# Kernel tuning notes

Hardware: AMD Instinct MI355X
Metric: run time of the kernel (lower is better)

The kernel has to match this reference:

```python
import jax, jax.numpy as jnp
import numpy as np

B = 16384      # rays
H = 128        # field hidden dim


def setup_inputs() -> dict:
    key = jax.random.key(0)
    ks = jax.random.split(key, 8)
    origins = jax.random.normal(ks[0], (B, 3), dtype=jnp.float32)
    directions = jax.random.normal(ks[1], (B, 3), dtype=jnp.float32)
    directions = directions / jnp.linalg.norm(directions, axis=-1, keepdims=True)
    # Field: simple MLP 3 -> H -> H -> 4 (rgb + sigma)
    W1 = jax.random.normal(ks[2], (3, H), dtype=jnp.float32) * (1.0 / np.sqrt(3.0))
    b1 = jnp.zeros((H,), dtype=jnp.float32)
    W2 = jax.random.normal(ks[3], (H, H), dtype=jnp.float32) * (1.0 / np.sqrt(H))
    b2 = jnp.zeros((H,), dtype=jnp.float32)
    W3 = jax.random.normal(ks[4], (H, 4), dtype=jnp.float32) * (1.0 / np.sqrt(H))
    b3 = jnp.zeros((4,), dtype=jnp.float32)
    return {"origins": origins, "directions": directions,
            "W1": W1, "b1": b1, "W2": W2, "b2": b2, "W3": W3, "b3": b3,
            "near": 2, "far": 6, "num_samples": 64}


def _field(x, W1, b1, W2, b2, W3, b3):
    h = jax.nn.relu(x @ W1 + b1)
    h = jax.nn.relu(h @ W2 + b2)
    return h @ W3 + b3


def reference(origins, directions, W1, b1, W2, b2, W3, b3, near, far, num_samples):
    near = jnp.float32(near)
    far = jnp.float32(far)
    # 1. generate_samples: segment boundaries + midpoints along each ray
    depths = jnp.linspace(near, far, num_samples + 1)            # [S+1]
    midpoints = 0.5 * (depths[:-1] + depths[1:])                 # [S]
    # [B, S, 3] = origin + t * direction
    locs = origins[:, None, :] + midpoints[None, :, None] * directions[:, None, :]
    # 2. evaluate field
    f = _field(locs.reshape(-1, 3), W1, b1, W2, b2, W3, b3)
    f = f.reshape(origins.shape[0], num_samples, 4)
    # NOTE: source overwrites the sigmoid'd colors with raw outputs (faithful)
    colors = f[..., :3]                                          # [B, S, 3]
    sigma = f[..., 3]                                            # [B, S]
    # 3. alpha values
    delta = depths[1:] - depths[:-1]                             # [S]
    alphas = 1.0 - jnp.exp(-sigma * delta[None, :])              # [B, S]
    # 4. alpha compositing (black background)
    ones = jnp.ones_like(alphas[:, :1])
    transmittance = jnp.cumprod(jnp.concatenate([ones, 1.0 - alphas], axis=1), axis=1)[:, :-1]
    weights = alphas * transmittance                             # [B, S]
    radiance = jnp.sum(weights[..., None] * colors, axis=1)      # [B, 3]
    return radiance
```

## Files before the change

### kernel.cpp

```cpp
#include <hip/hip_runtime.h>


typedef _Float16 f16;
typedef __attribute__((ext_vector_type(2))) _Float16 h2v;
typedef __attribute__((ext_vector_type(8))) _Float16 half8;
typedef __attribute__((ext_vector_type(4))) float floatx4;

#define H 128
#define NS 64

static __device__ __forceinline__ h2v pkrtz(float a, float b) {
  return __builtin_bit_cast(h2v, __builtin_amdgcn_cvt_pkrtz(a, b));
}

__global__ void nerf_setup(const float* __restrict__ W2, const float* __restrict__ W3,
                           const float* __restrict__ b2,
                           f16* __restrict__ wsW2, f16* __restrict__ wsW3,
                           f16* __restrict__ wsB2) {
  int t = blockIdx.x * blockDim.x + threadIdx.x;
  if (t < 8192) {
    int j2 = t & 3, lane = (t >> 2) & 63, fid = t >> 8;
    int mtl = fid & 1, ks = (fid >> 1) & 3, wv = fid >> 3;
    int l16 = lane & 15;
    int k = ks * 32 + ((lane >> 4) * 8) + 2 * j2;
    int n = 32 * wv + (l16 >> 2) * 8 + mtl * 4 + (l16 & 3);
    wsW2[2 * t]     = (f16)W2[k * H + n];
    wsW2[2 * t + 1] = (f16)W2[(k + 1) * H + n];
  } else if (t < 9216) {
    int u = t - 8192;
    int j2 = u & 3, lane = (u >> 2) & 63, wv = u >> 8;
    int c = lane & 15;
    int k3 = 32 * wv + ((lane >> 4) * 8) + 2 * j2;
    wsW3[2 * u]     = (c < 4) ? (f16)W3[k3 * 4 + c]       : (f16)0.0f;
    wsW3[2 * u + 1] = (c < 4) ? (f16)W3[(k3 + 1) * 4 + c] : (f16)0.0f;
  } else if (t < 9344) {
    int i = t - 9216;
    wsB2[i] = (f16)b2[i];
  }
}

__global__ __launch_bounds__(256, 3) void nerf_main(
    const float* __restrict__ origins, const float* __restrict__ dirs,
    const float* __restrict__ W1, const float* __restrict__ b1,
    const float* __restrict__ b3,
    const f16* __restrict__ wsW2, const f16* __restrict__ wsW3,
    const f16* __restrict__ wsB2,
    float* __restrict__ out)
{
  __shared__ __align__(16) f16   popd[2][2][H];
  __shared__ __align__(16) float f_lds[4][128][4];

  const int t = threadIdx.x;
  const int w = t >> 6, lane = t & 63, quad = lane >> 4, l16 = lane & 15;
  const float delta = 4.0f / NS;

  const half8* w2f = (const half8*)wsW2;
  half8 aw[4][2];
  #pragma unroll
  for (int ks = 0; ks < 4; ++ks)
    #pragma unroll
    for (int mtl = 0; mtl < 2; ++mtl)
      aw[ks][mtl] = w2f[((w * 4 + ks) * 2 + mtl) * 64 + lane];
  const half8 w3 = ((const half8*)wsW3)[w * 64 + lane];
  h2v bk[4];
  {
    uint4 u = *(const uint4*)(wsB2 + 32 * w + quad * 8);
    bk[0] = __builtin_bit_cast(h2v, u.x);
    bk[1] = __builtin_bit_cast(h2v, u.y);
    bk[2] = __builtin_bit_cast(h2v, u.z);
    bk[3] = __builtin_bit_cast(h2v, u.w);
  }
  const float4 b3v = *(const float4*)b3;

  if (w < 2) {
    const int ray = blockIdx.x * 2 + w;
    const float o0 = origins[ray*3], o1 = origins[ray*3+1], o2 = origins[ray*3+2];
    const float d0 = dirs[ray*3],    d1 = dirs[ray*3+1],    d2 = dirs[ray*3+2];
    const int k0 = lane * 2;
    const float2 wr0 = *(const float2*)&W1[0*H + k0];
    const float2 wr1 = *(const float2*)&W1[1*H + k0];
    const float2 wr2 = *(const float2*)&W1[2*H + k0];
    const float2 bb  = *(const float2*)&b1[k0];
    float poa = fmaf(o2, wr2.x, fmaf(o1, wr1.x, fmaf(o0, wr0.x, bb.x)));
    float pob = fmaf(o2, wr2.y, fmaf(o1, wr1.y, fmaf(o0, wr0.y, bb.y)));
    float pda = fmaf(d2, wr2.x, fmaf(d1, wr1.x, d0 * wr0.x));
    float pdb = fmaf(d2, wr2.y, fmaf(d1, wr1.y, d0 * wr0.y));
    h2v po2; po2[0] = (f16)poa; po2[1] = (f16)pob;
    h2v pd2; pd2[0] = (f16)pda; pd2[1] = (f16)pdb;
    *(h2v*)&popd[w][0][k0] = po2;
    *(h2v*)&popd[w][1][k0] = pd2;
  }
  __syncthreads();

  h2v m2[8];
  #pragma unroll
  for (int nt = 0; nt < 8; ++nt) {
    const f16 m = (f16)(2.0f + ((nt & 3) * 16 + l16 + 0.5f) * delta);
    m2[nt][0] = m; m2[nt][1] = m;
  }

  floatx4 acc[2][8];
  #pragma unroll
  for (int nt = 0; nt < 8; ++nt) { acc[0][nt] = (floatx4)(0.0f); acc[1][nt] = (floatx4)(0.0f); }

  const h2v z2 = (h2v)(f16)0.0f;
  #pragma unroll
  for (int ks = 0; ks < 4; ++ks) {
    const half8 poA = *(const half8*)&popd[0][0][ks*32 + quad*8];
    const half8 pdA = *(const half8*)&popd[0][1][ks*32 + quad*8];
    const half8 poB = *(const half8*)&popd[1][0][ks*32 + quad*8];
    const half8 pdB = *(const half8*)&popd[1][1][ks*32 + quad*8];
    #pragma unroll
    for (int nt = 0; nt < 8; ++nt) {
      union { half8 v; h2v p[4]; } P, O, Hb;
      P.v = (nt < 4) ? pdA : pdB;
      O.v = (nt < 4) ? poA : poB;
      #pragma unroll
      for (int p2 = 0; p2 < 4; ++p2)
        Hb.p[p2] = __builtin_elementwise_max((h2v)(P.p[p2] * m2[nt] + O.p[p2]), z2);
      acc[0][nt] = __builtin_amdgcn_mfma_f32_16x16x32_f16(aw[ks][0], Hb.v, acc[0][nt], 0, 0, 0);
      acc[1][nt] = __builtin_amdgcn_mfma_f32_16x16x32_f16(aw[ks][1], Hb.v, acc[1][nt], 0, 0, 0);
    }
  }

  #pragma unroll
  for (int nt = 0; nt < 8; ++nt) {
    h2v c0 = __builtin_elementwise_max((h2v)(pkrtz(acc[0][nt][0], acc[0][nt][1]) + bk[0]), z2);
    h2v c1 = __builtin_elementwise_max((h2v)(pkrtz(acc[0][nt][2], acc[0][nt][3]) + bk[1]), z2);
    h2v c2 = __builtin_elementwise_max((h2v)(pkrtz(acc[1][nt][0], acc[1][nt][1]) + bk[2]), z2);
    h2v c3 = __builtin_elementwise_max((h2v)(pkrtz(acc[1][nt][2], acc[1][nt][3]) + bk[3]), z2);
    half8 b = { c0[0], c0[1], c1[0], c1[1], c2[0], c2[1], c3[0], c3[1] };
    floatx4 d = __builtin_amdgcn_mfma_f32_16x16x32_f16(w3, b, (floatx4)(0.0f), 0, 0, 0);
    if (quad == 0) {
      float4 fv; fv.x = d[0]; fv.y = d[1]; fv.z = d[2]; fv.w = d[3];
      *(float4*)&f_lds[w][nt*16 + l16][0] = fv;
    }
  }
  __syncthreads();

  if (w < 2) {
    const int p = w * 64 + lane;
    const float4 s0 = *(const float4*)&f_lds[0][p][0];
    const float4 s1 = *(const float4*)&f_lds[1][p][0];
    const float4 s2 = *(const float4*)&f_lds[2][p][0];
    const float4 s3 = *(const float4*)&f_lds[3][p][0];
    const float fr = s0.x + s1.x + s2.x + s3.x + b3v.x;
    const float fg = s0.y + s1.y + s2.y + s3.y + b3v.y;
    const float fb = s0.z + s1.z + s2.z + s3.z + b3v.z;
    const float sigma = s0.w + s1.w + s2.w + s3.w + b3v.w;

    const float alpha = 1.0f - __expf(-sigma * delta);
    float S = sigma;
    #pragma unroll
    for (int off = 1; off < 64; off <<= 1) {
      float u = __shfl_up(S, off);
      if (lane >= off) S += u;
    }
    const float T  = __expf(-delta * (S - sigma));
    const float wt = alpha * T;
    float cr = wt * fr, cg = wt * fg, cb = wt * fb;
    #pragma unroll
    for (int off = 32; off > 0; off >>= 1) {
      cr += __shfl_down(cr, off);
      cg += __shfl_down(cg, off);
      cb += __shfl_down(cb, off);
    }
    if (lane == 0) {
      const int ray = blockIdx.x * 2 + w;
      out[ray*3+0] = cr; out[ray*3+1] = cg; out[ray*3+2] = cb;
    }
  }
}

extern "C" void kernel_launch(void* const* d_in, const int* in_sizes, int n_in,
                              void* d_out, int out_size, void* d_ws, size_t ws_size,
                              hipStream_t stream) {
  const float* origins = (const float*)d_in[0];
  const float* dirs    = (const float*)d_in[1];
  const float* W1      = (const float*)d_in[2];
  const float* b1      = (const float*)d_in[3];
  const float* W2      = (const float*)d_in[4];
  const float* b2      = (const float*)d_in[5];
  const float* W3      = (const float*)d_in[6];
  const float* b3      = (const float*)d_in[7];
  float* out = (float*)d_out;

  f16* wsW2 = (f16*)d_ws;
  f16* wsW3 = wsW2 + 16384;
  f16* wsB2 = wsW3 + 2048;

  nerf_setup<<<37, 256, 0, stream>>>(W2, W3, b2, wsW2, wsW3, wsB2);
  nerf_main<<<16384 / 2, 256, 0, stream>>>(
      origins, dirs, W1, b1, b3, wsW2, wsW3, wsB2, out);
}
```

Before: 117.2 us.

## Make nerf_main a persistent grid-stride kernel over ray pairs

Launches a fixed grid of 768 blocks, which matches 3 blocks per CU from the launch bounds on 256 CUs, and loops each block over ray pairs. The W2/W3 fragments, biases and W1 columns are then loaded into registers once per block instead of once per ray pair, which removes repeated setup and launch overhead for 8192 blocks. The inner MFMA loop is also split into two halves so the second ray's LDS fragments are loaded only when needed, which may lower register pressure. The trade-off is that each iteration still needs two block barriers, and with a fixed grid there is less freedom to hide latency across independent blocks.

```diff
diff --git a/kernel.cpp b/kernel.cpp
--- a/kernel.cpp
+++ b/kernel.cpp
@@ -8,6 +8,8 @@
 
 #define H 128
 #define NS 64
+#define NBLK 768
+#define RAYPAIRS 8192
 
 static __device__ __forceinline__ h2v pkrtz(float a, float b) {
   return __builtin_bit_cast(h2v, __builtin_amdgcn_cvt_pkrtz(a, b));
@@ -71,103 +73,113 @@
     bk[3] = __builtin_bit_cast(h2v, u.w);
   }
   const float4 b3v = *(const float4*)b3;
-
-  if (w < 2) {
-    const int ray = blockIdx.x * 2 + w;
-    const float o0 = origins[ray*3], o1 = origins[ray*3+1], o2 = origins[ray*3+2];
-    const float d0 = dirs[ray*3],    d1 = dirs[ray*3+1],    d2 = dirs[ray*3+2];
-    const int k0 = lane * 2;
-    const float2 wr0 = *(const float2*)&W1[0*H + k0];
-    const float2 wr1 = *(const float2*)&W1[1*H + k0];
-    const float2 wr2 = *(const float2*)&W1[2*H + k0];
-    const float2 bb  = *(const float2*)&b1[k0];
-    float poa = fmaf(o2, wr2.x, fmaf(o1, wr1.x, fmaf(o0, wr0.x, bb.x)));
-    float pob = fmaf(o2, wr2.y, fmaf(o1, wr1.y, fmaf(o0, wr0.y, bb.y)));
-    float pda = fmaf(d2, wr2.x, fmaf(d1, wr1.x, d0 * wr0.x));
-    float pdb = fmaf(d2, wr2.y, fmaf(d1, wr1.y, d0 * wr0.y));
-    h2v po2; po2[0] = (f16)poa; po2[1] = (f16)pob;
-    h2v pd2; pd2[0] = (f16)pda; pd2[1] = (f16)pdb;
-    *(h2v*)&popd[w][0][k0] = po2;
-    *(h2v*)&popd[w][1][k0] = pd2;
-  }
-  __syncthreads();
-
+  const int k0 = lane * 2;
+  const float2 wr0 = *(const float2*)&W1[0*H + k0];
+  const float2 wr1 = *(const float2*)&W1[1*H + k0];
+  const float2 wr2 = *(const float2*)&W1[2*H + k0];
+  const float2 bb  = *(const float2*)&b1[k0];
   h2v m2[8];
   #pragma unroll
   for (int nt = 0; nt < 8; ++nt) {
     const f16 m = (f16)(2.0f + ((nt & 3) * 16 + l16 + 0.5f) * delta);
     m2[nt][0] = m; m2[nt][1] = m;
   }
-
-  floatx4 acc[2][8];
-  #pragma unroll
-  for (int nt = 0; nt < 8; ++nt) { acc[0][nt] = (floatx4)(0.0f); acc[1][nt] = (floatx4)(0.0f); }
-
   const h2v z2 = (h2v)(f16)0.0f;
-  #pragma unroll
-  for (int ks = 0; ks < 4; ++ks) {
-    const half8 poA = *(const half8*)&popd[0][0][ks*32 + quad*8];
-    const half8 pdA = *(const half8*)&popd[0][1][ks*32 + quad*8];
-    const half8 poB = *(const half8*)&popd[1][0][ks*32 + quad*8];
-    const half8 pdB = *(const half8*)&popd[1][1][ks*32 + quad*8];
+
+  for (int p = blockIdx.x; p < RAYPAIRS; p += NBLK) {
+    if (w < 2) {
+      const int ray = 2 * p + w;
+      const float o0 = origins[ray*3], o1 = origins[ray*3+1], o2 = origins[ray*3+2];
+      const float d0 = dirs[ray*3],    d1 = dirs[ray*3+1],    d2 = dirs[ray*3+2];
+      float poa = fmaf(o2, wr2.x, fmaf(o1, wr1.x, fmaf(o0, wr0.x, bb.x)));
+      float pob = fmaf(o2, wr2.y, fmaf(o1, wr1.y, fmaf(o0, wr0.y, bb.y)));
+      float pda = fmaf(d2, wr2.x, fmaf(d1, wr1.x, d0 * wr0.x));
+      float pdb = fmaf(d2, wr2.y, fmaf(d1, wr1.y, d0 * wr0.y));
+      h2v po2; po2[0] = (f16)poa; po2[1] = (f16)pob;
+      h2v pd2; pd2[0] = (f16)pda; pd2[1] = (f16)pdb;
+      *(h2v*)&popd[w][0][k0] = po2;
+      *(h2v*)&popd[w][1][k0] = pd2;
+    }
+    __syncthreads();
+
+    floatx4 acc[2][8];
+    #pragma unroll
+    for (int nt = 0; nt < 8; ++nt) { acc[0][nt] = (floatx4)(0.0f); acc[1][nt] = (floatx4)(0.0f); }
+
+    #pragma unroll
+    for (int ks = 0; ks < 4; ++ks) {
+      const half8 poA = *(const half8*)&popd[0][0][ks*32 + quad*8];
+      const half8 pdA = *(const half8*)&popd[0][1][ks*32 + quad*8];
+      #pragma unroll
+      for (int nt = 0; nt < 4; ++nt) {
+        union { half8 v; h2v p[4]; } P, O, Hb;
+        P.v = pdA; O.v = poA;
+        #pragma unroll
+        for (int p2 = 0; p2 < 4; ++p2)
+          Hb.p[p2] = __builtin_elementwise_max((h2v)(P.p[p2] * m2[nt] + O.p[p2]), z2);
+        acc[0][nt] = __builtin_amdgcn_mfma_f32_16x16x32_f16(aw[ks][0], Hb.v, acc[0][nt], 0, 0, 0);
+        acc[1][nt] = __builtin_amdgcn_mfma_f32_16x16x32_f16(aw[ks][1], Hb.v, acc[1][nt], 0, 0, 0);
+      }
+      const half8 poB = *(const half8*)&popd[1][0][ks*32 + quad*8];
+      const half8 pdB = *(const half8*)&popd[1][1][ks*32 + quad*8];
+      #pragma unroll
+      for (int nt = 4; nt < 8; ++nt) {
+        union { half8 v; h2v p[4]; } P, O, Hb;
+        P.v = pdB; O.v = poB;
+        #pragma unroll
+        for (int p2 = 0; p2 < 4; ++p2)
+          Hb.p[p2] = __builtin_elementwise_max((h2v)(P.p[p2] * m2[nt] + O.p[p2]), z2);
+        acc[0][nt] = __builtin_amdgcn_mfma_f32_16x16x32_f16(aw[ks][0], Hb.v, acc[0][nt], 0, 0, 0);
+        acc[1][nt] = __builtin_amdgcn_mfma_f32_16x16x32_f16(aw[ks][1], Hb.v, acc[1][nt], 0, 0, 0);
+      }
+    }
+
     #pragma unroll
     for (int nt = 0; nt < 8; ++nt) {
-      union { half8 v; h2v p[4]; } P, O, Hb;
-      P.v = (nt < 4) ? pdA : pdB;
-      O.v = (nt < 4) ? poA : poB;
-      #pragma unroll
-      for (int p2 = 0; p2 < 4; ++p2)
-        Hb.p[p2] = __builtin_elementwise_max((h2v)(P.p[p2] * m2[nt] + O.p[p2]), z2);
-      acc[0][nt] = __builtin_amdgcn_mfma_f32_16x16x32_f16(aw[ks][0], Hb.v, acc[0][nt], 0, 0, 0);
-      acc[1][nt] = __builtin_amdgcn_mfma_f32_16x16x32_f16(aw[ks][1], Hb.v, acc[1][nt], 0, 0, 0);
-    }
-  }
-
-  #pragma unroll
-  for (int nt = 0; nt < 8; ++nt) {
-    h2v c0 = __builtin_elementwise_max((h2v)(pkrtz(acc[0][nt][0], acc[0][nt][1]) + bk[0]), z2);
-    h2v c1 = __builtin_elementwise_max((h2v)(pkrtz(acc[0][nt][2], acc[0][nt][3]) + bk[1]), z2);
-    h2v c2 = __builtin_elementwise_max((h2v)(pkrtz(acc[1][nt][0], acc[1][nt][1]) + bk[2]), z2);
-    h2v c3 = __builtin_elementwise_max((h2v)(pkrtz(acc[1][nt][2], acc[1][nt][3]) + bk[3]), z2);
-    half8 b = { c0[0], c0[1], c1[0], c1[1], c2[0], c2[1], c3[0], c3[1] };
-    floatx4 d = __builtin_amdgcn_mfma_f32_16x16x32_f16(w3, b, (floatx4)(0.0f), 0, 0, 0);
-    if (quad == 0) {
-      float4 fv; fv.x = d[0]; fv.y = d[1]; fv.z = d[2]; fv.w = d[3];
-      *(float4*)&f_lds[w][nt*16 + l16][0] = fv;
-    }
-  }
-  __syncthreads();
-
-  if (w < 2) {
-    const int p = w * 64 + lane;
-    const float4 s0 = *(const float4*)&f_lds[0][p][0];
-    const float4 s1 = *(const float4*)&f_lds[1][p][0];
-    const float4 s2 = *(const float4*)&f_lds[2][p][0];
-    const float4 s3 = *(const float4*)&f_lds[3][p][0];
-    const float fr = s0.x + s1.x + s2.x + s3.x + b3v.x;
-    const float fg = s0.y + s1.y + s2.y + s3.y + b3v.y;
-    const float fb = s0.z + s1.z + s2.z + s3.z + b3v.z;
-    const float sigma = s0.w + s1.w + s2.w + s3.w + b3v.w;
-
-    const float alpha = 1.0f - __expf(-sigma * delta);
-    float S = sigma;
-    #pragma unroll
-    for (int off = 1; off < 64; off <<= 1) {
-      float u = __shfl_up(S, off);
-      if (lane >= off) S += u;
-    }
-    const float T  = __expf(-delta * (S - sigma));
-    const float wt = alpha * T;
-    float cr = wt * fr, cg = wt * fg, cb = wt * fb;
-    #pragma unroll
-    for (int off = 32; off > 0; off >>= 1) {
-      cr += __shfl_down(cr, off);
-      cg += __shfl_down(cg, off);
-      cb += __shfl_down(cb, off);
-    }
-    if (lane == 0) {
-      const int ray = blockIdx.x * 2 + w;
-      out[ray*3+0] = cr; out[ray*3+1] = cg; out[ray*3+2] = cb;
+      h2v c0 = __builtin_elementwise_max((h2v)(pkrtz(acc[0][nt][0], acc[0][nt][1]) + bk[0]), z2);
+      h2v c1 = __builtin_elementwise_max((h2v)(pkrtz(acc[0][nt][2], acc[0][nt][3]) + bk[1]), z2);
+      h2v c2 = __builtin_elementwise_max((h2v)(pkrtz(acc[1][nt][0], acc[1][nt][1]) + bk[2]), z2);
+      h2v c3 = __builtin_elementwise_max((h2v)(pkrtz(acc[1][nt][2], acc[1][nt][3]) + bk[3]), z2);
+      half8 b = { c0[0], c0[1], c1[0], c1[1], c2[0], c2[1], c3[0], c3[1] };
+      floatx4 d = __builtin_amdgcn_mfma_f32_16x16x32_f16(w3, b, (floatx4)(0.0f), 0, 0, 0);
+      if (quad == 0) {
+        float4 fv; fv.x = d[0]; fv.y = d[1]; fv.z = d[2]; fv.w = d[3];
+        *(float4*)&f_lds[w][nt*16 + l16][0] = fv;
+      }
+    }
+    __syncthreads();
+
+    if (w < 2) {
+      const int pt = w * 64 + lane;
+      const float4 s0 = *(const float4*)&f_lds[0][pt][0];
+      const float4 s1 = *(const float4*)&f_lds[1][pt][0];
+      const float4 s2 = *(const float4*)&f_lds[2][pt][0];
+      const float4 s3 = *(const float4*)&f_lds[3][pt][0];
+      const float fr = s0.x + s1.x + s2.x + s3.x + b3v.x;
+      const float fg = s0.y + s1.y + s2.y + s3.y + b3v.y;
+      const float fb = s0.z + s1.z + s2.z + s3.z + b3v.z;
+      const float sigma = s0.w + s1.w + s2.w + s3.w + b3v.w;
+
+      const float alpha = 1.0f - __expf(-sigma * delta);
+      float S = sigma;
+      #pragma unroll
+      for (int off = 1; off < 64; off <<= 1) {
+        float u = __shfl_up(S, off);
+        if (lane >= off) S += u;
+      }
+      const float T  = __expf(-delta * (S - sigma));
+      const float wt = alpha * T;
+      float cr = wt * fr, cg = wt * fg, cb = wt * fb;
+      #pragma unroll
+      for (int off = 32; off > 0; off >>= 1) {
+        cr += __shfl_down(cr, off);
+        cg += __shfl_down(cg, off);
+        cb += __shfl_down(cb, off);
+      }
+      if (lane == 0) {
+        const int ray = 2 * p + w;
+        out[ray*3+0] = cr; out[ray*3+1] = cg; out[ray*3+2] = cb;
+      }
     }
   }
 }
@@ -190,6 +202,6 @@
   f16* wsB2 = wsW3 + 2048;
 
   nerf_setup<<<37, 256, 0, stream>>>(W2, W3, b2, wsW2, wsW3, wsB2);
-  nerf_main<<<16384 / 2, 256, 0, stream>>>(
+  nerf_main<<<NBLK, 256, 0, stream>>>(
       origins, dirs, W1, b1, b3, wsW2, wsW3, wsB2, out);
 }
```

Result: slower. 126.4 us (+7.8%).
